# Performance work log

Measured on AMD Instinct MI355X. Metric: run time of the kernel, lower is better.

The kernel has to match this reference:

```python
import jax, jax.numpy as jnp
import numpy as np

S = 8      # max segment id present in masks
D = 768    # hidden size (hardcoded in the torch module)
N_VIS = 100  # leading vision tokens in vision_trace_feat


def _segment_mean(feat, mask, n_seg):
    """Per-(batch, seg_id) mean of feat tokens where mask == seg_id.
    feat: [B, L, D], mask: [B, L] ints in 0..n_seg. Returns means [B, n_seg, D], counts [B, n_seg].
    Equivalent to the torch loop over seg_id + split + per-chunk mean(dim=0)."""
    onehot = (mask[:, :, None] == jnp.arange(1, n_seg + 1)[None, None, :]).astype(feat.dtype)  # [B,L,S]
    sums = jnp.einsum('bls,bld->bsd', onehot, feat)   # [B,S,D]
    counts = onehot.sum(axis=1)                        # [B,S]
    means = sums / jnp.maximum(counts, 1.0)[:, :, None]
    return means, counts


def setup_inputs() -> dict:
    key = jax.random.key(0)
    k1, k2, k3, k4, k5, k6 = jax.random.split(key, 6)
    B = 64
    vision_trace_feat = jax.random.normal(k1, (B, N_VIS + 412, D), dtype=jnp.float32)
    vision_trace_mask = jnp.sort(jax.random.randint(k2, (B, 412), 0, S + 1), axis=-1).astype(jnp.int32)
    caption_feat = jax.random.normal(k3, (B, 512, D), dtype=jnp.float32)
    caption_mask = jnp.sort(jax.random.randint(k4, (B, 513), 0, S + 1), axis=-1).astype(jnp.int32)
    vt_merge_w = jax.random.normal(k5, (2 * D, D), dtype=jnp.float32) * 0.02
    vt_merge_b = jax.random.normal(k6, (D,), dtype=jnp.float32) * 0.02
    return {
        'vision_trace_feat': vision_trace_feat,
        'vision_trace_mask': vision_trace_mask,
        'caption_feat': caption_feat,
        'caption_mask': caption_mask,
        'vt_merge_w': vt_merge_w,
        'vt_merge_b': vt_merge_b,
    }


def reference(vision_trace_feat, vision_trace_mask, caption_feat, caption_mask, vt_merge_w, vt_merge_b):
    # --- CaptionAggregator (meanpool) ---
    cm = caption_mask[:, 1:]                                   # drop CLS position
    c_means, c_counts = _segment_mean(caption_feat, cm, S)      # [B,S,D], [B,S]
    c_present = (c_counts > 0).astype(c_means.dtype)
    caption_out = c_means * c_present[:, :, None]               # dense form: empty segments zeroed

    # --- VisionTraceAggregator (meanpool) ---
    vision_feat = vision_trace_feat[:, :N_VIS].mean(axis=1)     # [B,D]
    trace_feat = vision_trace_feat[:, N_VIS:]                   # [B,Lt,D]
    t_means, t_counts = _segment_mean(trace_feat, vision_trace_mask, S)
    t_present = (t_counts > 0).astype(t_means.dtype)
    vt = jnp.concatenate(
        [t_means, jnp.broadcast_to(vision_feat[:, None, :], t_means.shape)], axis=-1)  # [B,S,2D]
    vt_out = (vt @ vt_merge_w + vt_merge_b) * t_present[:, :, None]
    return (caption_out, vt_out)
```

## Files before the change

kernel.cpp:

```cpp
#include <hip/hip_runtime.h>
#include <hip/hip_bf16.h>

#define SEGS   8
#define DIM    768
#define NVIS   100
#define BATCH  64
#define LTOK   512
#define NCHK   8
#define TPC    64

#define OFF_PCAP  0
#define OFF_PTRC  (OFF_PCAP + BATCH*NCHK*SEGS*DIM)
#define OFF_PVIS  (OFF_PTRC + BATCH*NCHK*SEGS*DIM)
#define OFF_PCCNT (OFF_PVIS + BATCH*2*DIM)
#define OFF_PTCNT (OFF_PCCNT + BATCH*NCHK*SEGS)
#define OFF_TMEAN (OFF_PTCNT + BATCH*NCHK*SEGS)
#define OFF_TCNT  (OFF_TMEAN + BATCH*9*DIM)


__global__ __launch_bounds__(192) void reduce_kernel(
    const float* __restrict__ vt_feat,
    const int* __restrict__ vt_mask,
    const float* __restrict__ cap_feat,
    const int* __restrict__ cap_mask,
    float* __restrict__ ws)
{
    const int bid  = blockIdx.x;
    const int type = bid >> 10;
    const int b    = (bid >> 4) & 63;
    const int ck   = (bid >> 1) & 7;
    const int half = bid & 1;
    const int tid  = threadIdx.x;
    const int c0   = half * 384 + tid * 2;

    __shared__ __align__(16) int msk[TPC];
    __shared__ int scnt[SEGS + 1];
    if (tid < SEGS + 1) scnt[tid] = 0;
    if (tid < TPC) {
        const int l = ck * TPC + tid;
        int m;
        if (type == 0) m = cap_mask[b * 513 + 1 + l];
        else           m = (l >= NVIS) ? vt_mask[b * 412 + (l - NVIS)] : 0;
        msk[tid] = m;
    }
    __syncthreads();
    if (half == 0 && tid < TPC) {
        const int m = msk[tid]; if (m > 0) atomicAdd(&scnt[m], 1);
    }

    float acc[SEGS][2];
#pragma unroll
    for (int s = 0; s < SEGS; ++s) { acc[s][0] = 0.f; acc[s][1] = 0.f; }
    float vacc[2] = {0.f, 0.f};
    float tmp[2]  = {0.f, 0.f};
    int cur = 0;

    const float* __restrict__ feat = (type == 0) ? cap_feat : vt_feat;
    const size_t base = (size_t)b * LTOK * DIM + (size_t)c0;

    for (int j = 0; j < TPC; j += 8) {
        const float* p = feat + base + (size_t)(ck * TPC + j) * DIM;
        float2 v[8];
#pragma unroll
        for (int u = 0; u < 8; ++u)
            v[u] = *reinterpret_cast<const float2*>(p + (size_t)u * DIM);
        const int4 m4a = *reinterpret_cast<const int4*>(&msk[j]);
        const int4 m4b = *reinterpret_cast<const int4*>(&msk[j + 4]);
        const int mm[8] = {m4a.x, m4a.y, m4a.z, m4a.w,
                           m4b.x, m4b.y, m4b.z, m4b.w};
#pragma unroll
        for (int u = 0; u < 8; ++u) {
            const int l = ck * TPC + j + u;
            if (type == 1 && l < NVIS) {
                vacc[0] += v[u].x; vacc[1] += v[u].y;
            } else {
                const int m = __builtin_amdgcn_readfirstlane(mm[u]);
                if (m != cur) {
#pragma unroll
                    for (int s = 0; s < SEGS; ++s)
                        if (cur == s + 1) {
                            acc[s][0] += tmp[0]; acc[s][1] += tmp[1];
                        }
                    tmp[0] = 0.f; tmp[1] = 0.f;
                    cur = m;
                }
                tmp[0] += v[u].x; tmp[1] += v[u].y;
            }
        }
    }
#pragma unroll
    for (int s = 0; s < SEGS; ++s)
        if (cur == s + 1) {
            acc[s][0] += tmp[0]; acc[s][1] += tmp[1];
        }

    __syncthreads();

    float* __restrict__ pbase = ws + (type == 0 ? OFF_PCAP : OFF_PTRC)
                              + ((size_t)(b * NCHK + ck) * SEGS) * DIM + c0;
#pragma unroll
    for (int s = 0; s < SEGS; ++s) {
        *reinterpret_cast<float2*>(pbase + s * DIM) =
            make_float2(acc[s][0], acc[s][1]);
    }
    if (half == 0) {
        int* __restrict__ cbase = (int*)(ws + (type == 0 ? OFF_PCCNT : OFF_PTCNT))
                                + (b * NCHK + ck) * SEGS;
        if (tid < SEGS) cbase[tid] = scnt[tid + 1];
    }
    if (type == 1 && ck < 2) {
        *reinterpret_cast<float2*>(ws + OFF_PVIS + (size_t)(b * 2 + ck) * DIM + c0) =
            make_float2(vacc[0], vacc[1]);
    }
}

__global__ __launch_bounds__(256) void combine1_kernel(
    const float* __restrict__ ws_c, float* __restrict__ ws,
    float* __restrict__ out)
{
    const int i = blockIdx.x * 256 + threadIdx.x;
    const int N1 = BATCH * SEGS * DIM / 4;
    if (i < N1) {
        const int b  = i / 1536;
        const int r  = i % 1536;
        const int s  = r / 192;
        const int d4 = (r % 192) * 4;
        float4 sum = make_float4(0.f, 0.f, 0.f, 0.f); int c = 0;
#pragma unroll
        for (int ck = 0; ck < NCHK; ++ck) {
            const float4 v = *reinterpret_cast<const float4*>(
                ws_c + OFF_PCAP + ((size_t)((b * NCHK + ck) * SEGS + s)) * DIM + d4);
            sum.x += v.x; sum.y += v.y; sum.z += v.z; sum.w += v.w;
            c += ((const int*)(ws_c + OFF_PCCNT))[(b * NCHK + ck) * SEGS + s];
        }
        float4 o = make_float4(0.f, 0.f, 0.f, 0.f);
        if (c > 0) {
            const float fc = (float)c;
            o = make_float4(sum.x / fc, sum.y / fc, sum.z / fc, sum.w / fc);
        }
        reinterpret_cast<float4*>(out)[i] = o;
    } else if (i < 2 * N1) {
        const int j  = i - N1;
        const int b  = j / 1536;
        const int r  = j % 1536;
        const int s  = r / 192;
        const int d4 = (r % 192) * 4;
        float4 sum = make_float4(0.f, 0.f, 0.f, 0.f); int c = 0;
#pragma unroll
        for (int ck = 0; ck < NCHK; ++ck) {
            const float4 v = *reinterpret_cast<const float4*>(
                ws_c + OFF_PTRC + ((size_t)((b * NCHK + ck) * SEGS + s)) * DIM + d4);
            sum.x += v.x; sum.y += v.y; sum.z += v.z; sum.w += v.w;
            c += ((const int*)(ws_c + OFF_PTCNT))[(b * NCHK + ck) * SEGS + s];
        }
        float4 m = make_float4(0.f, 0.f, 0.f, 0.f);
        if (c > 0) {
            const float fc = (float)c;
            m = make_float4(sum.x / fc, sum.y / fc, sum.z / fc, sum.w / fc);
        }
        *reinterpret_cast<float4*>(ws + OFF_TMEAN + ((size_t)(b * 9 + s)) * DIM + d4) = m;
        if (d4 == 0) ((int*)(ws + OFF_TCNT))[b * SEGS + s] = c;
    } else {
        const int j  = i - 2 * N1;
        const int b  = j / 192;
        const int d4 = (j % 192) * 4;
        const float4 v0 = *reinterpret_cast<const float4*>(
            ws_c + OFF_PVIS + (size_t)(b * 2 + 0) * DIM + d4);
        const float4 v1 = *reinterpret_cast<const float4*>(
            ws_c + OFF_PVIS + (size_t)(b * 2 + 1) * DIM + d4);
        const float sc = 1.0f / (float)NVIS;
        *reinterpret_cast<float4*>(ws + OFF_TMEAN + ((size_t)(b * 9 + 8)) * DIM + d4) =
            make_float4((v0.x + v1.x) * sc, (v0.y + v1.y) * sc,
                        (v0.z + v1.z) * sc, (v0.w + v1.w) * sc);
    }
}

__global__ __launch_bounds__(192) void gemm2_kernel(
    const float* __restrict__ W,
    const float* __restrict__ bias,
    const float* __restrict__ ws_c,
    float* __restrict__ out)
{
    const int b   = blockIdx.x >> 3;
    const int nc  = blockIdx.x & 7;
    const int n0  = nc * 96;
    const int tid = threadIdx.x;
    const int cg  = tid % 24;
    const int kq  = tid / 24;
    const int d0  = n0 + cg * 4;

    __shared__ __align__(16) float tm[9 * 8 * 100];
    __shared__ __align__(16) float red[192 * 9 * 4];

    for (int idx = tid; idx < 9 * DIM / 4; idx += 192) {
        const int r   = idx / 192;
        const int rem = idx % 192;
        const int kq_ = rem / 24;
        const int kk4 = rem % 24;
        const float4 v = reinterpret_cast<const float4*>(
            ws_c + OFF_TMEAN + (size_t)b * 9 * DIM)[idx];
        *reinterpret_cast<float4*>(&tm[(r * 8 + kq_) * 100 + kk4 * 4]) = v;
    }
    __syncthreads();

    float acc[9][4];
#pragma unroll
    for (int r = 0; r < 9; ++r) { acc[r][0]=0.f; acc[r][1]=0.f; acc[r][2]=0.f; acc[r][3]=0.f; }

    const float* __restrict__ Wt = W + (size_t)(kq * 96) * DIM + d0;
    const float* __restrict__ Wb = W + (size_t)(DIM + kq * 96) * DIM + d0;

    for (int kk = 0; kk < 96; kk += 4) {
        float4 wt[4], wb[4];
#pragma unroll
        for (int u = 0; u < 4; ++u) {
            wt[u] = *reinterpret_cast<const float4*>(Wt + (size_t)(kk + u) * DIM);
            wb[u] = *reinterpret_cast<const float4*>(Wb + (size_t)(kk + u) * DIM);
        }
        float a[9][4];
#pragma unroll
        for (int r = 0; r < 9; ++r) {
            const float4 t = *reinterpret_cast<const float4*>(&tm[(r * 8 + kq) * 100 + kk]);
            a[r][0] = t.x; a[r][1] = t.y; a[r][2] = t.z; a[r][3] = t.w;
        }
#pragma unroll
        for (int u = 0; u < 4; ++u) {
            const float t4[4] = {wt[u].x, wt[u].y, wt[u].z, wt[u].w};
            const float b4[4] = {wb[u].x, wb[u].y, wb[u].z, wb[u].w};
#pragma unroll
            for (int r = 0; r < SEGS; ++r) {
#pragma unroll
                for (int j = 0; j < 4; ++j) acc[r][j] += a[r][u] * t4[j];
            }
#pragma unroll
            for (int j = 0; j < 4; ++j) acc[8][j] += a[8][u] * b4[j];
        }
    }

#pragma unroll
    for (int r = 0; r < 9; ++r)
        *reinterpret_cast<float4*>(&red[(tid * 9 + r) * 4]) =
            make_float4(acc[r][0], acc[r][1], acc[r][2], acc[r][3]);
    __syncthreads();

    {
        const int cg2 = tid >> 3;
        const int s   = tid & 7;
        float4 sumS = make_float4(0.f, 0.f, 0.f, 0.f);
        float4 sumV = make_float4(0.f, 0.f, 0.f, 0.f);
#pragma unroll
        for (int q = 0; q < 8; ++q) {
            const int base = (q * 24 + cg2) * 9;
            const float4 vS = *reinterpret_cast<const float4*>(&red[(base + s) * 4]);
            const float4 vV = *reinterpret_cast<const float4*>(&red[(base + 8) * 4]);
            sumS.x += vS.x; sumS.y += vS.y; sumS.z += vS.z; sumS.w += vS.w;
            sumV.x += vV.x; sumV.y += vV.y; sumV.z += vV.z; sumV.w += vV.w;
        }
        const int dd = n0 + cg2 * 4;
        const int c  = ((const int*)(ws_c + OFF_TCNT))[b * SEGS + s];
        float4 o = make_float4(0.f, 0.f, 0.f, 0.f);
        if (c > 0) {
            const float4 bb = *reinterpret_cast<const float4*>(bias + dd);
            o = make_float4(sumS.x + sumV.x + bb.x, sumS.y + sumV.y + bb.y,
                            sumS.z + sumV.z + bb.z, sumS.w + sumV.w + bb.w);
        }
        *reinterpret_cast<float4*>(out + (size_t)BATCH * SEGS * DIM
                                   + ((size_t)(b * SEGS + s)) * DIM + dd) = o;
    }
}

extern "C" void kernel_launch(void* const* d_in, const int* in_sizes, int n_in,
                              void* d_out, int out_size, void* d_ws, size_t ws_size,
                              hipStream_t stream) {
    const float* vt_feat  = (const float*)d_in[0];
    const int*   vt_mask  = (const int*)d_in[1];
    const float* cap_feat = (const float*)d_in[2];
    const int*   cap_mask = (const int*)d_in[3];
    const float* W        = (const float*)d_in[4];
    const float* bias     = (const float*)d_in[5];
    float* out = (float*)d_out;
    float* ws = (float*)d_ws;

    reduce_kernel  <<<2048, 192, 0, stream>>>(vt_feat, vt_mask, cap_feat, cap_mask, ws);
    combine1_kernel<<<816, 256, 0, stream>>>(ws, ws, out);
    gemm2_kernel   <<<512, 192, 0, stream>>>(W, bias, ws, out);
}
```

Measured before the change: 259.5 us.

## Split token chunk across two thread teams with float4 loads and LDS reduction

The reduce kernel now has each block handle the full 768-wide hidden dimension, with threads loading float4 instead of float2. The block's 64 tokens are split between two 192-thread teams of 32 tokens each. The partial sums are combined through shared memory before one team writes to the workspace. This halves the block count, widens memory transactions and shortens each thread's serial token loop, at the cost of an extra LDS reduction, a barrier and more shared memory per block.

```diff
diff --git a/kernel.cpp b/kernel.cpp
--- a/kernel.cpp
+++ b/kernel.cpp
@@ -18,7 +18,7 @@
 #define OFF_TCNT  (OFF_TMEAN + BATCH*9*DIM)
 
 
-__global__ __launch_bounds__(192) void reduce_kernel(
+__global__ __launch_bounds__(384) void reduce_kernel(
     const float* __restrict__ vt_feat,
     const int* __restrict__ vt_mask,
     const float* __restrict__ cap_feat,
@@ -26,15 +26,19 @@
     float* __restrict__ ws)
 {
     const int bid  = blockIdx.x;
-    const int type = bid >> 10;
-    const int b    = (bid >> 4) & 63;
-    const int ck   = (bid >> 1) & 7;
-    const int half = bid & 1;
+    const int type = bid >> 9;
+    const int b    = (bid >> 3) & 63;
+    const int ck   = bid & 7;
     const int tid  = threadIdx.x;
-    const int c0   = half * 384 + tid * 2;
+    const int team = tid / 192;
+    const int t    = tid % 192;
+    const int c0   = t * 4;
 
     __shared__ __align__(16) int msk[TPC];
     __shared__ int scnt[SEGS + 1];
+    __shared__ __align__(16) float4 red[SEGS][192];
+    __shared__ __align__(16) float4 redv[192];
+
     if (tid < SEGS + 1) scnt[tid] = 0;
     if (tid < TPC) {
         const int l = ck * TPC + tid;
@@ -44,35 +48,32 @@
         msk[tid] = m;
     }
     __syncthreads();
-    if (half == 0 && tid < TPC) {
-        const int m = msk[tid]; if (m > 0) atomicAdd(&scnt[m], 1);
-    }
-
-    float acc[SEGS][2];
-#pragma unroll
-    for (int s = 0; s < SEGS; ++s) { acc[s][0] = 0.f; acc[s][1] = 0.f; }
-    float vacc[2] = {0.f, 0.f};
-    float tmp[2]  = {0.f, 0.f};
+    if (tid < TPC) { const int m = msk[tid]; if (m > 0) atomicAdd(&scnt[m], 1); }
+
+    float acc[SEGS][4];
+#pragma unroll
+    for (int s = 0; s < SEGS; ++s) { acc[s][0]=0.f; acc[s][1]=0.f; acc[s][2]=0.f; acc[s][3]=0.f; }
+    float vacc[4] = {0.f, 0.f, 0.f, 0.f};
+    float tmp[4]  = {0.f, 0.f, 0.f, 0.f};
     int cur = 0;
 
     const float* __restrict__ feat = (type == 0) ? cap_feat : vt_feat;
+    const int tok0 = ck * TPC + team * 32;
     const size_t base = (size_t)b * LTOK * DIM + (size_t)c0;
 
-    for (int j = 0; j < TPC; j += 8) {
-        const float* p = feat + base + (size_t)(ck * TPC + j) * DIM;
-        float2 v[8];
-#pragma unroll
-        for (int u = 0; u < 8; ++u)
-            v[u] = *reinterpret_cast<const float2*>(p + (size_t)u * DIM);
-        const int4 m4a = *reinterpret_cast<const int4*>(&msk[j]);
-        const int4 m4b = *reinterpret_cast<const int4*>(&msk[j + 4]);
-        const int mm[8] = {m4a.x, m4a.y, m4a.z, m4a.w,
-                           m4b.x, m4b.y, m4b.z, m4b.w};
-#pragma unroll
-        for (int u = 0; u < 8; ++u) {
-            const int l = ck * TPC + j + u;
+    for (int j = 0; j < 32; j += 4) {
+        const float* p = feat + base + (size_t)(tok0 + j) * DIM;
+        float4 v[4];
+#pragma unroll
+        for (int u = 0; u < 4; ++u)
+            v[u] = *reinterpret_cast<const float4*>(p + (size_t)u * DIM);
+        const int4 m4 = *reinterpret_cast<const int4*>(&msk[team * 32 + j]);
+        const int mm[4] = {m4.x, m4.y, m4.z, m4.w};
+#pragma unroll
+        for (int u = 0; u < 4; ++u) {
+            const int l = tok0 + j + u;
             if (type == 1 && l < NVIS) {
-                vacc[0] += v[u].x; vacc[1] += v[u].y;
+                vacc[0] += v[u].x; vacc[1] += v[u].y; vacc[2] += v[u].z; vacc[3] += v[u].w;
             } else {
                 const int m = __builtin_amdgcn_readfirstlane(mm[u]);
                 if (m != cur) {
@@ -80,11 +81,12 @@
                     for (int s = 0; s < SEGS; ++s)
                         if (cur == s + 1) {
                             acc[s][0] += tmp[0]; acc[s][1] += tmp[1];
+                            acc[s][2] += tmp[2]; acc[s][3] += tmp[3];
                         }
-                    tmp[0] = 0.f; tmp[1] = 0.f;
+                    tmp[0] = 0.f; tmp[1] = 0.f; tmp[2] = 0.f; tmp[3] = 0.f;
                     cur = m;
                 }
-                tmp[0] += v[u].x; tmp[1] += v[u].y;
+                tmp[0] += v[u].x; tmp[1] += v[u].y; tmp[2] += v[u].z; tmp[3] += v[u].w;
             }
         }
     }
@@ -92,25 +94,38 @@
     for (int s = 0; s < SEGS; ++s)
         if (cur == s + 1) {
             acc[s][0] += tmp[0]; acc[s][1] += tmp[1];
-        }
-
+            acc[s][2] += tmp[2]; acc[s][3] += tmp[3];
+        }
+
+    if (team == 1) {
+#pragma unroll
+        for (int s = 0; s < SEGS; ++s)
+            red[s][t] = make_float4(acc[s][0], acc[s][1], acc[s][2], acc[s][3]);
+        redv[t] = make_float4(vacc[0], vacc[1], vacc[2], vacc[3]);
+    }
     __syncthreads();
 
-    float* __restrict__ pbase = ws + (type == 0 ? OFF_PCAP : OFF_PTRC)
-                              + ((size_t)(b * NCHK + ck) * SEGS) * DIM + c0;
-#pragma unroll
-    for (int s = 0; s < SEGS; ++s) {
-        *reinterpret_cast<float2*>(pbase + s * DIM) =
-            make_float2(acc[s][0], acc[s][1]);
-    }
-    if (half == 0) {
-        int* __restrict__ cbase = (int*)(ws + (type == 0 ? OFF_PCCNT : OFF_PTCNT))
-                                + (b * NCHK + ck) * SEGS;
-        if (tid < SEGS) cbase[tid] = scnt[tid + 1];
-    }
-    if (type == 1 && ck < 2) {
-        *reinterpret_cast<float2*>(ws + OFF_PVIS + (size_t)(b * 2 + ck) * DIM + c0) =
-            make_float2(vacc[0], vacc[1]);
+    if (team == 0) {
+        float* __restrict__ pbase = ws + (type == 0 ? OFF_PCAP : OFF_PTRC)
+                                  + ((size_t)(b * NCHK + ck) * SEGS) * DIM + c0;
+#pragma unroll
+        for (int s = 0; s < SEGS; ++s) {
+            const float4 r1 = red[s][t];
+            *reinterpret_cast<float4*>(pbase + s * DIM) =
+                make_float4(acc[s][0] + r1.x, acc[s][1] + r1.y,
+                            acc[s][2] + r1.z, acc[s][3] + r1.w);
+        }
+        if (t < SEGS) {
+            int* __restrict__ cbase = (int*)(ws + (type == 0 ? OFF_PCCNT : OFF_PTCNT))
+                                    + (b * NCHK + ck) * SEGS;
+            cbase[t] = scnt[t + 1];
+        }
+        if (type == 1 && ck < 2) {
+            const float4 r1 = redv[t];
+            *reinterpret_cast<float4*>(ws + OFF_PVIS + (size_t)(b * 2 + ck) * DIM + c0) =
+                make_float4(vacc[0] + r1.x, vacc[1] + r1.y,
+                            vacc[2] + r1.z, vacc[3] + r1.w);
+        }
     }
 }
 
@@ -281,7 +296,7 @@
     float* out = (float*)d_out;
     float* ws = (float*)d_ws;
 
-    reduce_kernel  <<<2048, 192, 0, stream>>>(vt_feat, vt_mask, cap_feat, cap_mask, ws);
+    reduce_kernel  <<<1024, 384, 0, stream>>>(vt_feat, vt_mask, cap_feat, cap_mask, ws);
     combine1_kernel<<<816, 256, 0, stream>>>(ws, ws, out);
     gemm2_kernel   <<<512, 192, 0, stream>>>(W, bias, ws, out);
 }
```

New measurement: 260.6 us. Within noise of the previous version (+0.4%).
